# Kernel tuning notes

Measured on AMD Instinct MI355X. Metric: run time of the kernel, lower is better.

The kernel has to match this reference:

```python
import jax, jax.numpy as jnp
import numpy as np

N = 10000
E = 160000
UNITS = 64
NUM_RBF = 32
CUTOFF = 1.0


def _xavier(k, shape):
    fan_out, fan_in = shape
    lim = float(np.sqrt(6.0 / (fan_in + fan_out)))
    return jax.random.uniform(k, shape, minval=-lim, maxval=lim, dtype=jnp.float32)


def setup_inputs() -> dict:
    key = jax.random.key(0)
    ks = jax.random.split(key, 16)
    inp = {
        "edge_index": jax.random.randint(ks[0], (2, E), 0, N),
        "edge_weight": jax.random.uniform(ks[1], (E,), dtype=jnp.float32),
        "edge_attr": jax.random.normal(ks[2], (E, NUM_RBF), dtype=jnp.float32),
        "X": jax.random.normal(ks[3], (N, UNITS, 3, 3), dtype=jnp.float32),
        # scalar MLP: num_rbf -> units -> 2*units -> 3*units
        "Ws0": _xavier(ks[4], (UNITS, NUM_RBF)), "bs0": jnp.zeros((UNITS,), jnp.float32),
        "Ws1": _xavier(ks[5], (2 * UNITS, UNITS)), "bs1": jnp.zeros((2 * UNITS,), jnp.float32),
        "Ws2": _xavier(ks[6], (3 * UNITS, 2 * UNITS)), "bs2": jnp.zeros((3 * UNITS,), jnp.float32),
    }
    for i in range(6):
        inp[f"Wt{i}"] = _xavier(ks[7 + i], (UNITS, UNITS))
    return inp


def cosine_cutoff(r, cutoff):
    return jnp.where(r < cutoff, 0.5 * (jnp.cos(jnp.pi * r / cutoff) + 1.0), 0.0)


def tensor_norm(X):
    # X: [N, units, 3, 3] -> [N, units]
    return jnp.sum(X * X, axis=(-2, -1))


def decompose_tensor(X):
    eye = jnp.eye(3, dtype=X.dtype)
    trace = jnp.trace(X, axis1=-2, axis2=-1)  # [N, units]
    I = (trace / 3.0)[..., None, None] * eye
    A = 0.5 * (X - jnp.swapaxes(X, -2, -1))
    S = 0.5 * (X + jnp.swapaxes(X, -2, -1)) - I
    return I, A, S


def channel_linear(T, W):
    # linear over the channel dim: [N, c, 3, 3] x [d, c] -> [N, d, 3, 3]
    return jnp.einsum('ncij,dc->ndij', T, W)


def reference(edge_index, edge_weight, edge_attr, X,
              Ws0, bs0, Ws1, bs1, Ws2, bs2,
              Wt0, Wt1, Wt2, Wt3, Wt4, Wt5):
    act = jax.nn.silu
    C = cosine_cutoff(edge_weight, CUTOFF)  # [E]
    h = act(edge_attr @ Ws0.T + bs0)
    h = act(h @ Ws1.T + bs1)
    h = act(h @ Ws2.T + bs2)  # [E, 3*units]
    ea = (h * C[:, None]).reshape(h.shape[0], UNITS, 3)  # [E, units, 3]

    X = X / (tensor_norm(X) + 1.0)[..., None, None]
    I, A, S = decompose_tensor(X)
    I = channel_linear(I, Wt0)
    A = channel_linear(A, Wt1)
    S = channel_linear(S, Wt2)
    Y = I + A + S

    src, dst = edge_index[0], edge_index[1]
    n = X.shape[0]
    # message = per-edge radial scaling of gathered node tensors; aggregate at src
    Im = jax.ops.segment_sum(ea[..., 0, None, None] * I[dst], src, num_segments=n)
    Am = jax.ops.segment_sum(ea[..., 1, None, None] * A[dst], src, num_segments=n)
    Sm = jax.ops.segment_sum(ea[..., 2, None, None] * S[dst], src, num_segments=n)
    msg = Im + Am + Sm

    # O(3): symmetrized product of batched 3x3 matmuls
    AB = jnp.matmul(msg, Y) + jnp.matmul(Y, msg)
    I2, A2, S2 = decompose_tensor(AB)
    normp1 = (tensor_norm(I2 + A2 + S2) + 1.0)[..., None, None]
    I2 = channel_linear(I2 / normp1, Wt3)
    A2 = channel_linear(A2 / normp1, Wt4)
    S2 = channel_linear(S2 / normp1, Wt5)
    dX = I2 + A2 + S2
    return X + dX + jnp.matmul(dX, dX)
```

## Files before the change

kernel.cpp:

```cpp
#include <hip/hip_runtime.h>
#include <math.h>

#define NN 10000
#define EE 160000

#define OFF_WTT 0
#define OFF_PK  24576
#define OFF_B2P 41984
#define OFF_IASH 42176
#define OFF_EAH 3242176
#define OFF_INT 18602176

typedef __attribute__((ext_vector_type(8))) _Float16 h16x8;
typedef __attribute__((ext_vector_type(2))) __fp16 fp16x2_raw;
typedef __attribute__((ext_vector_type(4))) float f32x4;

__device__ __forceinline__ float silu_f(float x) {
    return x * __builtin_amdgcn_rcpf(1.0f + __expf(-x));
}
__device__ __forceinline__ unsigned int pkh(float a, float b) {
    union { fp16x2_raw h; unsigned int u; } cv;
    cv.h = __builtin_amdgcn_cvt_pkrtz(a, b);
    return cv.u;
}
__device__ __forceinline__ unsigned short f2h(float f) {
    union { _Float16 h; unsigned short u; } cv; cv.h = (_Float16)f; return cv.u;
}
__device__ __forceinline__ float h2f(unsigned short s) {
    union { unsigned short u; _Float16 h; } cv; cv.u = s; return (float)cv.h;
}
__device__ __forceinline__ float h2f_lo(unsigned int u) { return h2f((unsigned short)(u & 0xffffu)); }
__device__ __forceinline__ float h2f_hi(unsigned int u) { return h2f((unsigned short)(u >> 16)); }

__global__ void k_prep(const float* __restrict__ Wt0, const float* __restrict__ Wt1,
                       const float* __restrict__ Wt2, const float* __restrict__ Wt3,
                       const float* __restrict__ Wt4, const float* __restrict__ Wt5,
                       const float* __restrict__ Ws0, const float* __restrict__ Ws1,
                       const float* __restrict__ Ws2, const float* __restrict__ bs2,
                       const int* __restrict__ ei,
                       float* __restrict__ WtT, unsigned short* __restrict__ PK,
                       float* __restrict__ bs2p, int* __restrict__ counts) {
    int idx = blockIdx.x * 256 + threadIdx.x;
    if (idx < 24576) {
        int k = idx >> 12, r = idx & 4095;
        int c = r >> 6, d = r & 63;
        const float* W = (k == 0) ? Wt0 : (k == 1) ? Wt1 : (k == 2) ? Wt2
                       : (k == 3) ? Wt3 : (k == 4) ? Wt4 : Wt5;
        WtT[idx] = W[d * 64 + c];
    } else if (idx < 26624) {
        int q = idx - 24576;
        int ot = q >> 9, r = q & 511, lane = r >> 3, j = r & 7;
        int k = ((lane >> 4) * 8) + j, o = ot * 16 + (lane & 15);
        PK[q] = f2h(Ws0[o * 32 + k]);
    } else if (idx < 34816) {
        int q = idx - 24576;
        int i = q - 2048, ch = i >> 9, r = i & 511, lane = r >> 3, j = r & 7;
        int ot = ch >> 1, ks = ch & 1;
        int k = ks * 32 + (lane >> 4) * 8 + j, o = ot * 16 + (lane & 15);
        PK[q] = f2h(Ws1[o * 64 + k]);
    } else if (idx < 59392) {
        int q = idx - 24576;
        int i = q - 10240, ch = i >> 9, r = i & 511, lane = r >> 3, j = r & 7;
        int ot = ch >> 2, ks = ch & 3;
        int k = ks * 32 + (lane >> 4) * 8 + j;
        int op = ot * 16 + (lane & 15);
        int o = (op & 63) * 3 + (op >> 6);
        PK[q] = f2h(Ws2[o * 128 + k]);
    } else if (idx < 59584) {
        int op = idx - 59392;
        bs2p[op] = bs2[(op & 63) * 3 + (op >> 6)];
    } else if (idx < 59584 + EE) {
        int e = idx - 59584;
        atomicAdd(&counts[ei[e]], 1);
    }
}

__global__ __launch_bounds__(256) void k_scan(const int* __restrict__ counts,
                                              int* __restrict__ offsets) {
    __shared__ int sums[256];
    int t = threadIdx.x;
    int base = t * 40;
    int s = 0;
    if (base < NN) {
        const int4* p = (const int4*)(counts + base);
#pragma unroll
        for (int q = 0; q < 10; ++q) { int4 a = p[q]; s += a.x + a.y + a.z + a.w; }
    }
    sums[t] = s;
    __syncthreads();
    for (int off = 1; off < 256; off <<= 1) {
        int tmp = (t >= off) ? sums[t - off] : 0;
        __syncthreads();
        sums[t] += tmp;
        __syncthreads();
    }
    int run = sums[t] - s;
    if (base < NN) {
        const int4* p = (const int4*)(counts + base);
#pragma unroll
        for (int q = 0; q < 10; ++q) {
            int4 a = p[q];
            offsets[base + 4 * q + 0] = run; run += a.x;
            offsets[base + 4 * q + 1] = run; run += a.y;
            offsets[base + 4 * q + 2] = run; run += a.z;
            offsets[base + 4 * q + 3] = run; run += a.w;
        }
    }
    if (t == 255) offsets[NN] = run;
}

__global__ void k_fill(const int* __restrict__ ei, const int* __restrict__ offsets,
                       int* __restrict__ cursor, int* __restrict__ bucket,
                       int* __restrict__ dstp) {
    int e = blockIdx.x * 256 + threadIdx.x;
    if (e < EE) {
        int s = ei[e];
        int pos = offsets[s] + atomicAdd(&cursor[s], 1);
        bucket[pos] = e;
        dstp[pos] = ei[EE + e];
    }
}

__global__ __launch_bounds__(256) void k_nodeprep(const float* __restrict__ X,
                                                  const float* __restrict__ WtT,
                                                  unsigned int* __restrict__ IASu) {
    int t = threadIdx.x, w = t >> 6, c = t & 63;
    int n = blockIdx.x * 4 + w;
    __shared__ float XS[4][576];
    __shared__ float L[4][64][12];
    float* xs = XS[w];
#pragma unroll
    for (int i = 0; i < 9; i++) xs[c + 64 * i] = X[(size_t)n * 576 + c + 64 * i];
    __builtin_amdgcn_wave_barrier();
    float x[9];
#pragma unroll
    for (int j = 0; j < 9; j++) x[j] = xs[c * 9 + j];
    float nrm = 0.f;
#pragma unroll
    for (int j = 0; j < 9; j++) nrm += x[j] * x[j];
    float inv = __builtin_amdgcn_rcpf(nrm + 1.0f);
#pragma unroll
    for (int j = 0; j < 9; j++) x[j] *= inv;
    float tr3 = (x[0] + x[4] + x[8]) * (1.0f / 3.0f);
    L[w][c][0] = tr3;
    L[w][c][1] = 0.5f * (x[1] - x[3]);
    L[w][c][2] = 0.5f * (x[2] - x[6]);
    L[w][c][3] = 0.5f * (x[5] - x[7]);
    L[w][c][4] = x[0] - tr3;
    L[w][c][5] = x[4] - tr3;
    L[w][c][6] = 0.5f * (x[1] + x[3]);
    L[w][c][7] = 0.5f * (x[2] + x[6]);
    L[w][c][8] = 0.5f * (x[5] + x[7]);
    __builtin_amdgcn_wave_barrier();
    int d = c;
    const float* W0 = WtT;
    const float* W1 = WtT + 4096;
    const float* W2 = WtT + 8192;
    float aI = 0, aA0 = 0, aA1 = 0, aA2 = 0, aS0 = 0, aS1 = 0, aS2 = 0, aS3 = 0, aS4 = 0;
    for (int cc = 0; cc < 64; ++cc) {
        float w0 = W0[cc * 64 + d], w1 = W1[cc * 64 + d], w2 = W2[cc * 64 + d];
        float4 L0 = *(const float4*)&L[w][cc][0];
        float4 L1 = *(const float4*)&L[w][cc][4];
        float L8 = L[w][cc][8];
        aI  += w0 * L0.x;
        aA0 += w1 * L0.y; aA1 += w1 * L0.z; aA2 += w1 * L0.w;
        aS0 += w2 * L1.x; aS1 += w2 * L1.y; aS2 += w2 * L1.z;
        aS3 += w2 * L1.w; aS4 += w2 * L8;
    }
    unsigned int* op = IASu + (size_t)n * 320 + d;
    op[0]   = pkh(aI, aA0);
    op[64]  = pkh(aA1, aA2);
    op[128] = pkh(aS0, aS1);
    op[192] = pkh(aS2, aS3);
    op[256] = pkh(aS4, 0.0f);
}

__global__ __launch_bounds__(256) void k_mlp(const float* __restrict__ attr,
                                             const float* __restrict__ ew,
                                             const int* __restrict__ bucket,
                                             const unsigned short* __restrict__ PK,
                                             const float* __restrict__ bs0,
                                             const float* __restrict__ bs1,
                                             const float* __restrict__ bs2p,
                                             unsigned short* __restrict__ eah) {
    __shared__ unsigned short H[4][2][16][136];
    int t = threadIdx.x;
    int l = t & 63, w = t >> 6, lr = l & 15, lg = l >> 4;
    int base = blockIdx.x * 128 + w * 32;
    const h16x8* P1 = (const h16x8*)PK;
    const h16x8* P2 = (const h16x8*)(PK + 2048);
    const h16x8* P3 = (const h16x8*)(PK + 10240);

    union { h16x8 h; unsigned int u[4]; } B1[2];
    float C[2];
#pragma unroll
    for (int tt = 0; tt < 2; ++tt) {
        int eid = bucket[base + tt * 16 + lr];
        const float* ap = attr + (size_t)eid * 32 + lg * 8;
        float4 a0 = *(const float4*)ap;
        float4 a1 = *(const float4*)(ap + 4);
        B1[tt].u[0] = pkh(a0.x, a0.y); B1[tt].u[1] = pkh(a0.z, a0.w);
        B1[tt].u[2] = pkh(a1.x, a1.y); B1[tt].u[3] = pkh(a1.z, a1.w);
        float rw = ew[eid];
        C[tt] = (rw < 1.0f) ? 0.5f * (cosf(3.14159265358979f * rw) + 1.0f) : 0.0f;
    }

#pragma unroll
    for (int ot = 0; ot < 4; ++ot) {
        h16x8 wf = P1[ot * 64 + l];
        float4 bb = *(const float4*)&bs0[ot * 16 + lg * 4];
#pragma unroll
        for (int tt = 0; tt < 2; ++tt) {
            f32x4 acc = {bb.x, bb.y, bb.z, bb.w};
            acc = __builtin_amdgcn_mfma_f32_16x16x32_f16(wf, B1[tt].h, acc, 0, 0, 0);
            unsigned int u01 = pkh(silu_f(acc[0]), silu_f(acc[1]));
            unsigned int u23 = pkh(silu_f(acc[2]), silu_f(acc[3]));
            *(uint2*)&H[w][tt][lr][ot * 16 + lg * 4] = make_uint2(u01, u23);
        }
    }
    __builtin_amdgcn_wave_barrier();

    h16x8 B2a[2], B2b[2];
#pragma unroll
    for (int tt = 0; tt < 2; ++tt) {
        B2a[tt] = *(const h16x8*)&H[w][tt][lr][lg * 8];
        B2b[tt] = *(const h16x8*)&H[w][tt][lr][32 + lg * 8];
    }
    __builtin_amdgcn_wave_barrier();
#pragma unroll
    for (int ot = 0; ot < 8; ++ot) {
        h16x8 wf0 = P2[(ot * 2 + 0) * 64 + l];
        h16x8 wf1 = P2[(ot * 2 + 1) * 64 + l];
        float4 bb = *(const float4*)&bs1[ot * 16 + lg * 4];
#pragma unroll
        for (int tt = 0; tt < 2; ++tt) {
            f32x4 acc = {bb.x, bb.y, bb.z, bb.w};
            acc = __builtin_amdgcn_mfma_f32_16x16x32_f16(wf0, B2a[tt], acc, 0, 0, 0);
            acc = __builtin_amdgcn_mfma_f32_16x16x32_f16(wf1, B2b[tt], acc, 0, 0, 0);
            unsigned int u01 = pkh(silu_f(acc[0]), silu_f(acc[1]));
            unsigned int u23 = pkh(silu_f(acc[2]), silu_f(acc[3]));
            *(uint2*)&H[w][tt][lr][ot * 16 + lg * 4] = make_uint2(u01, u23);
        }
    }
    __builtin_amdgcn_wave_barrier();

    h16x8 B3[4][2];
#pragma unroll
    for (int ks = 0; ks < 4; ++ks)
#pragma unroll
        for (int tt = 0; tt < 2; ++tt)
            B3[ks][tt] = *(const h16x8*)&H[w][tt][lr][ks * 32 + lg * 8];
#pragma unroll
    for (int ot = 0; ot < 12; ++ot) {
        h16x8 wf0 = P3[(ot * 4 + 0) * 64 + l];
        h16x8 wf1 = P3[(ot * 4 + 1) * 64 + l];
        h16x8 wf2 = P3[(ot * 4 + 2) * 64 + l];
        h16x8 wf3 = P3[(ot * 4 + 3) * 64 + l];
        float4 bb = *(const float4*)&bs2p[ot * 16 + lg * 4];
#pragma unroll
        for (int tt = 0; tt < 2; ++tt) {
            f32x4 acc = {bb.x, bb.y, bb.z, bb.w};
            acc = __builtin_amdgcn_mfma_f32_16x16x32_f16(wf0, B3[0][tt], acc, 0, 0, 0);
            acc = __builtin_amdgcn_mfma_f32_16x16x32_f16(wf1, B3[1][tt], acc, 0, 0, 0);
            acc = __builtin_amdgcn_mfma_f32_16x16x32_f16(wf2, B3[2][tt], acc, 0, 0, 0);
            acc = __builtin_amdgcn_mfma_f32_16x16x32_f16(wf3, B3[3][tt], acc, 0, 0, 0);
            unsigned int u01 = pkh(silu_f(acc[0]) * C[tt], silu_f(acc[1]) * C[tt]);
            unsigned int u23 = pkh(silu_f(acc[2]) * C[tt], silu_f(acc[3]) * C[tt]);
            *(uint2*)&eah[(size_t)(base + tt * 16 + lr) * 192 + ot * 16 + lg * 4]
                = make_uint2(u01, u23);
        }
    }
}

__global__ __launch_bounds__(256) void k_aggout(const int* __restrict__ offsets,
                                                const int* __restrict__ dstp,
                                                const unsigned short* __restrict__ eah,
                                                const unsigned int* __restrict__ IASu,
                                                const float* __restrict__ X,
                                                const float* __restrict__ WtT,
                                                float* __restrict__ out) {
    int t = threadIdx.x, w = t >> 6, c = t & 63;
    int n = blockIdx.x * 4 + w;
    __shared__ float XS[4][576];
    __shared__ float LO[4][768];
    float* xs = XS[w];
    float* lo = LO[w];
#pragma unroll
    for (int i = 0; i < 9; i++) xs[c + 64 * i] = X[(size_t)n * 576 + c + 64 * i];

    int beg = offsets[n], end = offsets[n + 1];
    float m0 = 0, m1 = 0, m2 = 0, m3 = 0, m4 = 0, m5 = 0, m6 = 0, m7 = 0, m8 = 0;
    int i = beg;
    for (; i + 2 <= end; i += 2) {
        int d0 = dstp[i], d1 = dstp[i + 1];
        const unsigned short* ep0 = eah + (size_t)i * 192;
        const unsigned short* ep1 = ep0 + 192;
        float a00 = h2f(ep0[c]), a01 = h2f(ep0[64 + c]), a02 = h2f(ep0[128 + c]);
        float a10 = h2f(ep1[c]), a11 = h2f(ep1[64 + c]), a12 = h2f(ep1[128 + c]);
        const unsigned int* p0 = IASu + (size_t)d0 * 320 + c;
        const unsigned int* p1 = IASu + (size_t)d1 * 320 + c;
        unsigned int u00 = p0[0], u01 = p0[64], u02 = p0[128], u03 = p0[192], u04 = p0[256];
        unsigned int u10 = p1[0], u11 = p1[64], u12 = p1[128], u13 = p1[192], u14 = p1[256];
        m0 += a00 * h2f_lo(u00) + a10 * h2f_lo(u10);
        m1 += a01 * h2f_hi(u00) + a11 * h2f_hi(u10);
        m2 += a01 * h2f_lo(u01) + a11 * h2f_lo(u11);
        m3 += a01 * h2f_hi(u01) + a11 * h2f_hi(u11);
        m4 += a02 * h2f_lo(u02) + a12 * h2f_lo(u12);
        m5 += a02 * h2f_hi(u02) + a12 * h2f_hi(u12);
        m6 += a02 * h2f_lo(u03) + a12 * h2f_lo(u13);
        m7 += a02 * h2f_hi(u03) + a12 * h2f_hi(u13);
        m8 += a02 * h2f_lo(u04) + a12 * h2f_lo(u14);
    }
    if (i < end) {
        int d0 = dstp[i];
        const unsigned short* ep0 = eah + (size_t)i * 192;
        float a00 = h2f(ep0[c]), a01 = h2f(ep0[64 + c]), a02 = h2f(ep0[128 + c]);
        const unsigned int* p0 = IASu + (size_t)d0 * 320 + c;
        unsigned int u00 = p0[0], u01 = p0[64], u02 = p0[128], u03 = p0[192], u04 = p0[256];
        m0 += a00 * h2f_lo(u00); m1 += a01 * h2f_hi(u00);
        m2 += a01 * h2f_lo(u01); m3 += a01 * h2f_hi(u01);
        m4 += a02 * h2f_lo(u02); m5 += a02 * h2f_hi(u02);
        m6 += a02 * h2f_lo(u03); m7 += a02 * h2f_hi(u03);
        m8 += a02 * h2f_lo(u04);
    }
    const unsigned int* yp = IASu + (size_t)n * 320 + c;
    unsigned int y0 = yp[0], y1 = yp[64], y2 = yp[128], y3 = yp[192], y4 = yp[256];
    float yI = h2f_lo(y0), yA0 = h2f_hi(y0), yA1 = h2f_lo(y1), yA2 = h2f_hi(y1);
    float yS0 = h2f_lo(y2), yS1 = h2f_hi(y2), yS2 = h2f_lo(y3), yS3 = h2f_hi(y3);
    float yS4 = h2f_lo(y4);

    float M[3][3] = {
        { m0 + m4,   m1 + m6,  m2 + m7 },
        { -m1 + m6,  m0 + m5,  m3 + m8 },
        { -m2 + m7, -m3 + m8,  m0 - m4 - m5 } };
    float Y[3][3] = {
        { yI + yS0,   yA0 + yS2,  yA1 + yS3 },
        { -yA0 + yS2, yI + yS1,   yA2 + yS4 },
        { -yA1 + yS3, -yA2 + yS4, yI - yS0 - yS1 } };
    float AB[3][3];
#pragma unroll
    for (int ii = 0; ii < 3; ii++)
#pragma unroll
        for (int j = 0; j < 3; j++) {
            float s = 0.f;
#pragma unroll
            for (int k = 0; k < 3; k++) s += M[ii][k] * Y[k][j] + Y[ii][k] * M[k][j];
            AB[ii][j] = s;
        }
    float tr3 = (AB[0][0] + AB[1][1] + AB[2][2]) * (1.0f / 3.0f);
    float fro = 0.f;
#pragma unroll
    for (int ii = 0; ii < 3; ii++)
#pragma unroll
        for (int j = 0; j < 3; j++) fro += AB[ii][j] * AB[ii][j];
    float inv = __builtin_amdgcn_rcpf(fro + 1.0f);
    float (*L12)[12] = (float (*)[12])lo;
    L12[c][0] = tr3 * inv;
    L12[c][1] = 0.5f * (AB[0][1] - AB[1][0]) * inv;
    L12[c][2] = 0.5f * (AB[0][2] - AB[2][0]) * inv;
    L12[c][3] = 0.5f * (AB[1][2] - AB[2][1]) * inv;
    L12[c][4] = (AB[0][0] - tr3) * inv;
    L12[c][5] = (AB[1][1] - tr3) * inv;
    L12[c][6] = 0.5f * (AB[0][1] + AB[1][0]) * inv;
    L12[c][7] = 0.5f * (AB[0][2] + AB[2][0]) * inv;
    L12[c][8] = 0.5f * (AB[1][2] + AB[2][1]) * inv;
    __builtin_amdgcn_wave_barrier();
    int d = c;
    const float* W3 = WtT + 3 * 4096;
    const float* W4 = WtT + 4 * 4096;
    const float* W5 = WtT + 5 * 4096;
    float aI = 0, aA0 = 0, aA1 = 0, aA2 = 0, aS0 = 0, aS1 = 0, aS2 = 0, aS3 = 0, aS4 = 0;
    for (int cc = 0; cc < 64; ++cc) {
        float w3 = W3[cc * 64 + d], w4 = W4[cc * 64 + d], w5 = W5[cc * 64 + d];
        float4 L0 = *(const float4*)&L12[cc][0];
        float4 L1 = *(const float4*)&L12[cc][4];
        float L8 = L12[cc][8];
        aI  += w3 * L0.x;
        aA0 += w4 * L0.y; aA1 += w4 * L0.z; aA2 += w4 * L0.w;
        aS0 += w5 * L1.x; aS1 += w5 * L1.y; aS2 += w5 * L1.z;
        aS3 += w5 * L1.w; aS4 += w5 * L8;
    }
    float dX[3][3] = {
        { aI + aS0,   aA0 + aS2,  aA1 + aS3 },
        { -aA0 + aS2, aI + aS1,   aA2 + aS4 },
        { -aA1 + aS3, -aA2 + aS4, aI - aS0 - aS1 } };
    float D2[3][3];
#pragma unroll
    for (int ii = 0; ii < 3; ii++)
#pragma unroll
        for (int j = 0; j < 3; j++) {
            float s = 0.f;
#pragma unroll
            for (int k = 0; k < 3; k++) s += dX[ii][k] * dX[k][j];
            D2[ii][j] = s;
        }
    float x[9];
    __builtin_amdgcn_wave_barrier();
#pragma unroll
    for (int j = 0; j < 9; j++) x[j] = xs[d * 9 + j];
    float nrm = 0.f;
#pragma unroll
    for (int j = 0; j < 9; j++) nrm += x[j] * x[j];
    float xinv = __builtin_amdgcn_rcpf(nrm + 1.0f);
    __builtin_amdgcn_wave_barrier();
#pragma unroll
    for (int ii = 0; ii < 3; ii++)
#pragma unroll
        for (int j = 0; j < 3; j++)
            lo[d * 9 + ii * 3 + j] = x[ii * 3 + j] * xinv + dX[ii][j] + D2[ii][j];
    __builtin_amdgcn_wave_barrier();
#pragma unroll
    for (int ii = 0; ii < 9; ii++) out[(size_t)n * 576 + c + 64 * ii] = lo[c + 64 * ii];
}

extern "C" void kernel_launch(void* const* d_in, const int* in_sizes, int n_in,
                              void* d_out, int out_size, void* d_ws, size_t ws_size,
                              hipStream_t stream) {
    (void)in_sizes; (void)n_in; (void)out_size; (void)ws_size;
    const int* ei = (const int*)d_in[0];
    const float* ew = (const float*)d_in[1];
    const float* attr = (const float*)d_in[2];
    const float* X = (const float*)d_in[3];
    const float* Ws0 = (const float*)d_in[4];
    const float* bs0 = (const float*)d_in[5];
    const float* Ws1 = (const float*)d_in[6];
    const float* bs1 = (const float*)d_in[7];
    const float* Ws2 = (const float*)d_in[8];
    const float* bs2 = (const float*)d_in[9];
    const float* Wt0 = (const float*)d_in[10];
    const float* Wt1 = (const float*)d_in[11];
    const float* Wt2 = (const float*)d_in[12];
    const float* Wt3 = (const float*)d_in[13];
    const float* Wt4 = (const float*)d_in[14];
    const float* Wt5 = (const float*)d_in[15];
    float* ws = (float*)d_ws;
    int* ibase = (int*)(ws + OFF_INT);
    int* counts = ibase;
    int* cursor = ibase + NN;
    int* offsets = ibase + 2 * NN;
    int* bucket = ibase + 3 * NN + 1;
    int* dstp = bucket + EE;
    unsigned short* PK = (unsigned short*)(ws + OFF_PK);
    unsigned int* IASu = (unsigned int*)(ws + OFF_IASH);
    unsigned short* eah = (unsigned short*)(ws + OFF_EAH);

    (void)hipMemsetAsync(counts, 0, 2 * NN * sizeof(int), stream);
    k_prep<<<(59584 + EE + 255) / 256, 256, 0, stream>>>(
        Wt0, Wt1, Wt2, Wt3, Wt4, Wt5, Ws0, Ws1, Ws2, bs2, ei,
        ws, PK, ws + OFF_B2P, counts);
    k_scan<<<1, 256, 0, stream>>>(counts, offsets);
    k_fill<<<(EE + 255) / 256, 256, 0, stream>>>(ei, offsets, cursor, bucket, dstp);
    k_nodeprep<<<NN / 4, 256, 0, stream>>>(X, ws, IASu);
    k_mlp<<<EE / 128, 256, 0, stream>>>(attr, ew, bucket, PK, bs0, bs1, ws + OFF_B2P, eah);
    k_aggout<<<NN / 4, 256, 0, stream>>>(offsets, dstp, eah, IASu, X, ws, (float*)d_out);
}
```

Baseline: 151.5 us.

## Permute edge attrs in fill, merge nodeprep into MLP kernel, unroll aggregation by 4

The fill kernel now writes fp16-packed edge attributes and the cosine cutoff directly in bucket-sorted order, so the MLP reads contiguous rows instead of gathering through a bucket index. The node-prep work becomes extra blocks of the MLP launch, which saves one kernel launch and lets the two independent stages share the GPU. The aggregation loop is unrolled by four so more gathers are in flight at once. In exchange, fill does more scattered writes and the workspace holds an extra permuted attribute buffer.

```diff
diff --git a/kernel.cpp b/kernel.cpp
--- a/kernel.cpp
+++ b/kernel.cpp
@@ -9,7 +9,9 @@
 #define OFF_B2P 41984
 #define OFF_IASH 42176
 #define OFF_EAH 3242176
-#define OFF_INT 18602176
+#define OFF_ATTRP 18602176
+#define OFF_CP  21162176
+#define OFF_INT 21322176
 
 typedef __attribute__((ext_vector_type(8))) _Float16 h16x8;
 typedef __attribute__((ext_vector_type(2))) __fp16 fp16x2_raw;
@@ -110,165 +112,170 @@
 }
 
 __global__ void k_fill(const int* __restrict__ ei, const int* __restrict__ offsets,
-                       int* __restrict__ cursor, int* __restrict__ bucket,
-                       int* __restrict__ dstp) {
+                       const float* __restrict__ attr, const float* __restrict__ ew,
+                       int* __restrict__ cursor, int* __restrict__ dstp,
+                       unsigned short* __restrict__ attrP, float* __restrict__ Cp) {
     int e = blockIdx.x * 256 + threadIdx.x;
     if (e < EE) {
         int s = ei[e];
         int pos = offsets[s] + atomicAdd(&cursor[s], 1);
-        bucket[pos] = e;
         dstp[pos] = ei[EE + e];
-    }
-}
-
-__global__ __launch_bounds__(256) void k_nodeprep(const float* __restrict__ X,
-                                                  const float* __restrict__ WtT,
-                                                  unsigned int* __restrict__ IASu) {
-    int t = threadIdx.x, w = t >> 6, c = t & 63;
-    int n = blockIdx.x * 4 + w;
-    __shared__ float XS[4][576];
-    __shared__ float L[4][64][12];
-    float* xs = XS[w];
-#pragma unroll
-    for (int i = 0; i < 9; i++) xs[c + 64 * i] = X[(size_t)n * 576 + c + 64 * i];
-    __builtin_amdgcn_wave_barrier();
-    float x[9];
-#pragma unroll
-    for (int j = 0; j < 9; j++) x[j] = xs[c * 9 + j];
-    float nrm = 0.f;
-#pragma unroll
-    for (int j = 0; j < 9; j++) nrm += x[j] * x[j];
-    float inv = __builtin_amdgcn_rcpf(nrm + 1.0f);
-#pragma unroll
-    for (int j = 0; j < 9; j++) x[j] *= inv;
-    float tr3 = (x[0] + x[4] + x[8]) * (1.0f / 3.0f);
-    L[w][c][0] = tr3;
-    L[w][c][1] = 0.5f * (x[1] - x[3]);
-    L[w][c][2] = 0.5f * (x[2] - x[6]);
-    L[w][c][3] = 0.5f * (x[5] - x[7]);
-    L[w][c][4] = x[0] - tr3;
-    L[w][c][5] = x[4] - tr3;
-    L[w][c][6] = 0.5f * (x[1] + x[3]);
-    L[w][c][7] = 0.5f * (x[2] + x[6]);
-    L[w][c][8] = 0.5f * (x[5] + x[7]);
-    __builtin_amdgcn_wave_barrier();
-    int d = c;
-    const float* W0 = WtT;
-    const float* W1 = WtT + 4096;
-    const float* W2 = WtT + 8192;
-    float aI = 0, aA0 = 0, aA1 = 0, aA2 = 0, aS0 = 0, aS1 = 0, aS2 = 0, aS3 = 0, aS4 = 0;
-    for (int cc = 0; cc < 64; ++cc) {
-        float w0 = W0[cc * 64 + d], w1 = W1[cc * 64 + d], w2 = W2[cc * 64 + d];
-        float4 L0 = *(const float4*)&L[w][cc][0];
-        float4 L1 = *(const float4*)&L[w][cc][4];
-        float L8 = L[w][cc][8];
-        aI  += w0 * L0.x;
-        aA0 += w1 * L0.y; aA1 += w1 * L0.z; aA2 += w1 * L0.w;
-        aS0 += w2 * L1.x; aS1 += w2 * L1.y; aS2 += w2 * L1.z;
-        aS3 += w2 * L1.w; aS4 += w2 * L8;
-    }
-    unsigned int* op = IASu + (size_t)n * 320 + d;
-    op[0]   = pkh(aI, aA0);
-    op[64]  = pkh(aA1, aA2);
-    op[128] = pkh(aS0, aS1);
-    op[192] = pkh(aS2, aS3);
-    op[256] = pkh(aS4, 0.0f);
-}
-
-__global__ __launch_bounds__(256) void k_mlp(const float* __restrict__ attr,
-                                             const float* __restrict__ ew,
-                                             const int* __restrict__ bucket,
-                                             const unsigned short* __restrict__ PK,
-                                             const float* __restrict__ bs0,
-                                             const float* __restrict__ bs1,
-                                             const float* __restrict__ bs2p,
-                                             unsigned short* __restrict__ eah) {
-    __shared__ unsigned short H[4][2][16][136];
-    int t = threadIdx.x;
-    int l = t & 63, w = t >> 6, lr = l & 15, lg = l >> 4;
-    int base = blockIdx.x * 128 + w * 32;
-    const h16x8* P1 = (const h16x8*)PK;
-    const h16x8* P2 = (const h16x8*)(PK + 2048);
-    const h16x8* P3 = (const h16x8*)(PK + 10240);
-
-    union { h16x8 h; unsigned int u[4]; } B1[2];
-    float C[2];
-#pragma unroll
-    for (int tt = 0; tt < 2; ++tt) {
-        int eid = bucket[base + tt * 16 + lr];
-        const float* ap = attr + (size_t)eid * 32 + lg * 8;
-        float4 a0 = *(const float4*)ap;
-        float4 a1 = *(const float4*)(ap + 4);
-        B1[tt].u[0] = pkh(a0.x, a0.y); B1[tt].u[1] = pkh(a0.z, a0.w);
-        B1[tt].u[2] = pkh(a1.x, a1.y); B1[tt].u[3] = pkh(a1.z, a1.w);
-        float rw = ew[eid];
-        C[tt] = (rw < 1.0f) ? 0.5f * (cosf(3.14159265358979f * rw) + 1.0f) : 0.0f;
-    }
-
-#pragma unroll
-    for (int ot = 0; ot < 4; ++ot) {
-        h16x8 wf = P1[ot * 64 + l];
-        float4 bb = *(const float4*)&bs0[ot * 16 + lg * 4];
+        const float4* ap = (const float4*)(attr + (size_t)e * 32);
+        unsigned int pk[16];
+#pragma unroll
+        for (int q = 0; q < 8; ++q) {
+            float4 v = ap[q];
+            pk[2 * q]     = pkh(v.x, v.y);
+            pk[2 * q + 1] = pkh(v.z, v.w);
+        }
+        uint4* dst = (uint4*)(attrP + (size_t)pos * 32);
+#pragma unroll
+        for (int q = 0; q < 4; ++q)
+            dst[q] = make_uint4(pk[4 * q], pk[4 * q + 1], pk[4 * q + 2], pk[4 * q + 3]);
+        float rw = ew[e];
+        Cp[pos] = (rw < 1.0f) ? 0.5f * (cosf(3.14159265358979f * rw) + 1.0f) : 0.0f;
+    }
+}
+
+__global__ __launch_bounds__(256) void k_mlpnp(const unsigned short* __restrict__ attrP,
+                                               const float* __restrict__ Cp,
+                                               const unsigned short* __restrict__ PK,
+                                               const float* __restrict__ bs0,
+                                               const float* __restrict__ bs1,
+                                               const float* __restrict__ bs2p,
+                                               const float* __restrict__ X,
+                                               const float* __restrict__ WtT,
+                                               unsigned short* __restrict__ eah,
+                                               unsigned int* __restrict__ IASu) {
+    __shared__ unsigned short SH[4][4352];
+    int t = threadIdx.x, w = t >> 6, l = t & 63;
+    if (blockIdx.x < EE / 128) {
+        int lr = l & 15, lg = l >> 4;
+        int base = blockIdx.x * 128 + w * 32;
+        unsigned short* Hh = SH[w];
+        const h16x8* P1 = (const h16x8*)PK;
+        const h16x8* P2 = (const h16x8*)(PK + 2048);
+        const h16x8* P3 = (const h16x8*)(PK + 10240);
+        union { h16x8 h; uint4 v; } B1[2];
+        float C[2];
 #pragma unroll
         for (int tt = 0; tt < 2; ++tt) {
-            f32x4 acc = {bb.x, bb.y, bb.z, bb.w};
-            acc = __builtin_amdgcn_mfma_f32_16x16x32_f16(wf, B1[tt].h, acc, 0, 0, 0);
-            unsigned int u01 = pkh(silu_f(acc[0]), silu_f(acc[1]));
-            unsigned int u23 = pkh(silu_f(acc[2]), silu_f(acc[3]));
-            *(uint2*)&H[w][tt][lr][ot * 16 + lg * 4] = make_uint2(u01, u23);
-        }
-    }
-    __builtin_amdgcn_wave_barrier();
-
-    h16x8 B2a[2], B2b[2];
-#pragma unroll
-    for (int tt = 0; tt < 2; ++tt) {
-        B2a[tt] = *(const h16x8*)&H[w][tt][lr][lg * 8];
-        B2b[tt] = *(const h16x8*)&H[w][tt][lr][32 + lg * 8];
-    }
-    __builtin_amdgcn_wave_barrier();
-#pragma unroll
-    for (int ot = 0; ot < 8; ++ot) {
-        h16x8 wf0 = P2[(ot * 2 + 0) * 64 + l];
-        h16x8 wf1 = P2[(ot * 2 + 1) * 64 + l];
-        float4 bb = *(const float4*)&bs1[ot * 16 + lg * 4];
+            int p = base + tt * 16 + lr;
+            B1[tt].v = *((const uint4*)(attrP + (size_t)p * 32) + lg);
+            C[tt] = Cp[p];
+        }
+#pragma unroll
+        for (int ot = 0; ot < 4; ++ot) {
+            h16x8 wf = P1[ot * 64 + l];
+            float4 bb = *(const float4*)&bs0[ot * 16 + lg * 4];
+#pragma unroll
+            for (int tt = 0; tt < 2; ++tt) {
+                f32x4 acc = {bb.x, bb.y, bb.z, bb.w};
+                acc = __builtin_amdgcn_mfma_f32_16x16x32_f16(wf, B1[tt].h, acc, 0, 0, 0);
+                unsigned int u01 = pkh(silu_f(acc[0]), silu_f(acc[1]));
+                unsigned int u23 = pkh(silu_f(acc[2]), silu_f(acc[3]));
+                *(uint2*)&Hh[tt * 2176 + lr * 136 + ot * 16 + lg * 4] = make_uint2(u01, u23);
+            }
+        }
+        __builtin_amdgcn_wave_barrier();
+        h16x8 B2a[2], B2b[2];
 #pragma unroll
         for (int tt = 0; tt < 2; ++tt) {
-            f32x4 acc = {bb.x, bb.y, bb.z, bb.w};
-            acc = __builtin_amdgcn_mfma_f32_16x16x32_f16(wf0, B2a[tt], acc, 0, 0, 0);
-            acc = __builtin_amdgcn_mfma_f32_16x16x32_f16(wf1, B2b[tt], acc, 0, 0, 0);
-            unsigned int u01 = pkh(silu_f(acc[0]), silu_f(acc[1]));
-            unsigned int u23 = pkh(silu_f(acc[2]), silu_f(acc[3]));
-            *(uint2*)&H[w][tt][lr][ot * 16 + lg * 4] = make_uint2(u01, u23);
-        }
-    }
-    __builtin_amdgcn_wave_barrier();
-
-    h16x8 B3[4][2];
-#pragma unroll
-    for (int ks = 0; ks < 4; ++ks)
-#pragma unroll
-        for (int tt = 0; tt < 2; ++tt)
-            B3[ks][tt] = *(const h16x8*)&H[w][tt][lr][ks * 32 + lg * 8];
-#pragma unroll
-    for (int ot = 0; ot < 12; ++ot) {
-        h16x8 wf0 = P3[(ot * 4 + 0) * 64 + l];
-        h16x8 wf1 = P3[(ot * 4 + 1) * 64 + l];
-        h16x8 wf2 = P3[(ot * 4 + 2) * 64 + l];
-        h16x8 wf3 = P3[(ot * 4 + 3) * 64 + l];
-        float4 bb = *(const float4*)&bs2p[ot * 16 + lg * 4];
-#pragma unroll
-        for (int tt = 0; tt < 2; ++tt) {
-            f32x4 acc = {bb.x, bb.y, bb.z, bb.w};
-            acc = __builtin_amdgcn_mfma_f32_16x16x32_f16(wf0, B3[0][tt], acc, 0, 0, 0);
-            acc = __builtin_amdgcn_mfma_f32_16x16x32_f16(wf1, B3[1][tt], acc, 0, 0, 0);
-            acc = __builtin_amdgcn_mfma_f32_16x16x32_f16(wf2, B3[2][tt], acc, 0, 0, 0);
-            acc = __builtin_amdgcn_mfma_f32_16x16x32_f16(wf3, B3[3][tt], acc, 0, 0, 0);
-            unsigned int u01 = pkh(silu_f(acc[0]) * C[tt], silu_f(acc[1]) * C[tt]);
-            unsigned int u23 = pkh(silu_f(acc[2]) * C[tt], silu_f(acc[3]) * C[tt]);
-            *(uint2*)&eah[(size_t)(base + tt * 16 + lr) * 192 + ot * 16 + lg * 4]
-                = make_uint2(u01, u23);
-        }
+            B2a[tt] = *(const h16x8*)&Hh[tt * 2176 + lr * 136 + lg * 8];
+            B2b[tt] = *(const h16x8*)&Hh[tt * 2176 + lr * 136 + 32 + lg * 8];
+        }
+        __builtin_amdgcn_wave_barrier();
+#pragma unroll
+        for (int ot = 0; ot < 8; ++ot) {
+            h16x8 wf0 = P2[(ot * 2 + 0) * 64 + l];
+            h16x8 wf1 = P2[(ot * 2 + 1) * 64 + l];
+            float4 bb = *(const float4*)&bs1[ot * 16 + lg * 4];
+#pragma unroll
+            for (int tt = 0; tt < 2; ++tt) {
+                f32x4 acc = {bb.x, bb.y, bb.z, bb.w};
+                acc = __builtin_amdgcn_mfma_f32_16x16x32_f16(wf0, B2a[tt], acc, 0, 0, 0);
+                acc = __builtin_amdgcn_mfma_f32_16x16x32_f16(wf1, B2b[tt], acc, 0, 0, 0);
+                unsigned int u01 = pkh(silu_f(acc[0]), silu_f(acc[1]));
+                unsigned int u23 = pkh(silu_f(acc[2]), silu_f(acc[3]));
+                *(uint2*)&Hh[tt * 2176 + lr * 136 + ot * 16 + lg * 4] = make_uint2(u01, u23);
+            }
+        }
+        __builtin_amdgcn_wave_barrier();
+        h16x8 B3[4][2];
+#pragma unroll
+        for (int ks = 0; ks < 4; ++ks)
+#pragma unroll
+            for (int tt = 0; tt < 2; ++tt)
+                B3[ks][tt] = *(const h16x8*)&Hh[tt * 2176 + lr * 136 + ks * 32 + lg * 8];
+#pragma unroll
+        for (int ot = 0; ot < 12; ++ot) {
+            h16x8 wf0 = P3[(ot * 4 + 0) * 64 + l];
+            h16x8 wf1 = P3[(ot * 4 + 1) * 64 + l];
+            h16x8 wf2 = P3[(ot * 4 + 2) * 64 + l];
+            h16x8 wf3 = P3[(ot * 4 + 3) * 64 + l];
+            float4 bb = *(const float4*)&bs2p[ot * 16 + lg * 4];
+#pragma unroll
+            for (int tt = 0; tt < 2; ++tt) {
+                f32x4 acc = {bb.x, bb.y, bb.z, bb.w};
+                acc = __builtin_amdgcn_mfma_f32_16x16x32_f16(wf0, B3[0][tt], acc, 0, 0, 0);
+                acc = __builtin_amdgcn_mfma_f32_16x16x32_f16(wf1, B3[1][tt], acc, 0, 0, 0);
+                acc = __builtin_amdgcn_mfma_f32_16x16x32_f16(wf2, B3[2][tt], acc, 0, 0, 0);
+                acc = __builtin_amdgcn_mfma_f32_16x16x32_f16(wf3, B3[3][tt], acc, 0, 0, 0);
+                unsigned int u01 = pkh(silu_f(acc[0]) * C[tt], silu_f(acc[1]) * C[tt]);
+                unsigned int u23 = pkh(silu_f(acc[2]) * C[tt], silu_f(acc[3]) * C[tt]);
+                *(uint2*)&eah[(size_t)(base + tt * 16 + lr) * 192 + ot * 16 + lg * 4]
+                    = make_uint2(u01, u23);
+            }
+        }
+    } else {
+        int c = l;
+        int n = (blockIdx.x - EE / 128) * 4 + w;
+        float* xs = (float*)SH[w];
+        float (*L12)[12] = (float (*)[12])(xs + 576);
+#pragma unroll
+        for (int i = 0; i < 9; i++) xs[c + 64 * i] = X[(size_t)n * 576 + c + 64 * i];
+        __builtin_amdgcn_wave_barrier();
+        float x[9];
+#pragma unroll
+        for (int j = 0; j < 9; j++) x[j] = xs[c * 9 + j];
+        float nrm = 0.f;
+#pragma unroll
+        for (int j = 0; j < 9; j++) nrm += x[j] * x[j];
+        float inv = __builtin_amdgcn_rcpf(nrm + 1.0f);
+#pragma unroll
+        for (int j = 0; j < 9; j++) x[j] *= inv;
+        float tr3 = (x[0] + x[4] + x[8]) * (1.0f / 3.0f);
+        L12[c][0] = tr3;
+        L12[c][1] = 0.5f * (x[1] - x[3]);
+        L12[c][2] = 0.5f * (x[2] - x[6]);
+        L12[c][3] = 0.5f * (x[5] - x[7]);
+        L12[c][4] = x[0] - tr3;
+        L12[c][5] = x[4] - tr3;
+        L12[c][6] = 0.5f * (x[1] + x[3]);
+        L12[c][7] = 0.5f * (x[2] + x[6]);
+        L12[c][8] = 0.5f * (x[5] + x[7]);
+        __builtin_amdgcn_wave_barrier();
+        int d = c;
+        const float* W0 = WtT;
+        const float* W1 = WtT + 4096;
+        const float* W2 = WtT + 8192;
+        float aI = 0, aA0 = 0, aA1 = 0, aA2 = 0, aS0 = 0, aS1 = 0, aS2 = 0, aS3 = 0, aS4 = 0;
+        for (int cc = 0; cc < 64; ++cc) {
+            float w0 = W0[cc * 64 + d], w1 = W1[cc * 64 + d], w2 = W2[cc * 64 + d];
+            float4 L0 = *(const float4*)&L12[cc][0];
+            float4 L1 = *(const float4*)&L12[cc][4];
+            float L8 = L12[cc][8];
+            aI  += w0 * L0.x;
+            aA0 += w1 * L0.y; aA1 += w1 * L0.z; aA2 += w1 * L0.w;
+            aS0 += w2 * L1.x; aS1 += w2 * L1.y; aS2 += w2 * L1.z;
+            aS3 += w2 * L1.w; aS4 += w2 * L8;
+        }
+        unsigned int* op = IASu + (size_t)n * 320 + d;
+        op[0]   = pkh(aI, aA0);
+        op[64]  = pkh(aA1, aA2);
+        op[128] = pkh(aS0, aS1);
+        op[192] = pkh(aS2, aS3);
+        op[256] = pkh(aS4, 0.0f);
     }
 }
 
@@ -291,37 +298,35 @@
     int beg = offsets[n], end = offsets[n + 1];
     float m0 = 0, m1 = 0, m2 = 0, m3 = 0, m4 = 0, m5 = 0, m6 = 0, m7 = 0, m8 = 0;
     int i = beg;
-    for (; i + 2 <= end; i += 2) {
-        int d0 = dstp[i], d1 = dstp[i + 1];
-        const unsigned short* ep0 = eah + (size_t)i * 192;
-        const unsigned short* ep1 = ep0 + 192;
-        float a00 = h2f(ep0[c]), a01 = h2f(ep0[64 + c]), a02 = h2f(ep0[128 + c]);
-        float a10 = h2f(ep1[c]), a11 = h2f(ep1[64 + c]), a12 = h2f(ep1[128 + c]);
-        const unsigned int* p0 = IASu + (size_t)d0 * 320 + c;
-        const unsigned int* p1 = IASu + (size_t)d1 * 320 + c;
-        unsigned int u00 = p0[0], u01 = p0[64], u02 = p0[128], u03 = p0[192], u04 = p0[256];
-        unsigned int u10 = p1[0], u11 = p1[64], u12 = p1[128], u13 = p1[192], u14 = p1[256];
-        m0 += a00 * h2f_lo(u00) + a10 * h2f_lo(u10);
-        m1 += a01 * h2f_hi(u00) + a11 * h2f_hi(u10);
-        m2 += a01 * h2f_lo(u01) + a11 * h2f_lo(u11);
-        m3 += a01 * h2f_hi(u01) + a11 * h2f_hi(u11);
-        m4 += a02 * h2f_lo(u02) + a12 * h2f_lo(u12);
-        m5 += a02 * h2f_hi(u02) + a12 * h2f_hi(u12);
-        m6 += a02 * h2f_lo(u03) + a12 * h2f_lo(u13);
-        m7 += a02 * h2f_hi(u03) + a12 * h2f_hi(u13);
-        m8 += a02 * h2f_lo(u04) + a12 * h2f_lo(u14);
-    }
-    if (i < end) {
-        int d0 = dstp[i];
-        const unsigned short* ep0 = eah + (size_t)i * 192;
-        float a00 = h2f(ep0[c]), a01 = h2f(ep0[64 + c]), a02 = h2f(ep0[128 + c]);
-        const unsigned int* p0 = IASu + (size_t)d0 * 320 + c;
-        unsigned int u00 = p0[0], u01 = p0[64], u02 = p0[128], u03 = p0[192], u04 = p0[256];
-        m0 += a00 * h2f_lo(u00); m1 += a01 * h2f_hi(u00);
-        m2 += a01 * h2f_lo(u01); m3 += a01 * h2f_hi(u01);
-        m4 += a02 * h2f_lo(u02); m5 += a02 * h2f_hi(u02);
-        m6 += a02 * h2f_lo(u03); m7 += a02 * h2f_hi(u03);
-        m8 += a02 * h2f_lo(u04);
+    for (; i + 4 <= end; i += 4) {
+        float a[4][3];
+        unsigned int u[4][5];
+#pragma unroll
+        for (int q = 0; q < 4; ++q) {
+            const unsigned short* ep = eah + (size_t)(i + q) * 192;
+            a[q][0] = h2f(ep[c]); a[q][1] = h2f(ep[64 + c]); a[q][2] = h2f(ep[128 + c]);
+            const unsigned int* p = IASu + (size_t)dstp[i + q] * 320 + c;
+            u[q][0] = p[0]; u[q][1] = p[64]; u[q][2] = p[128]; u[q][3] = p[192]; u[q][4] = p[256];
+        }
+#pragma unroll
+        for (int q = 0; q < 4; ++q) {
+            m0 += a[q][0] * h2f_lo(u[q][0]); m1 += a[q][1] * h2f_hi(u[q][0]);
+            m2 += a[q][1] * h2f_lo(u[q][1]); m3 += a[q][1] * h2f_hi(u[q][1]);
+            m4 += a[q][2] * h2f_lo(u[q][2]); m5 += a[q][2] * h2f_hi(u[q][2]);
+            m6 += a[q][2] * h2f_lo(u[q][3]); m7 += a[q][2] * h2f_hi(u[q][3]);
+            m8 += a[q][2] * h2f_lo(u[q][4]);
+        }
+    }
+    for (; i < end; ++i) {
+        const unsigned short* ep = eah + (size_t)i * 192;
+        float a0 = h2f(ep[c]), a1 = h2f(ep[64 + c]), a2 = h2f(ep[128 + c]);
+        const unsigned int* p = IASu + (size_t)dstp[i] * 320 + c;
+        unsigned int u0 = p[0], u1 = p[64], u2 = p[128], u3 = p[192], u4 = p[256];
+        m0 += a0 * h2f_lo(u0); m1 += a1 * h2f_hi(u0);
+        m2 += a1 * h2f_lo(u1); m3 += a1 * h2f_hi(u1);
+        m4 += a2 * h2f_lo(u2); m5 += a2 * h2f_hi(u2);
+        m6 += a2 * h2f_lo(u3); m7 += a2 * h2f_hi(u3);
+        m8 += a2 * h2f_lo(u4);
     }
     const unsigned int* yp = IASu + (size_t)n * 320 + c;
     unsigned int y0 = yp[0], y1 = yp[64], y2 = yp[128], y3 = yp[192], y4 = yp[256];
@@ -438,19 +443,20 @@
     int* counts = ibase;
     int* cursor = ibase + NN;
     int* offsets = ibase + 2 * NN;
-    int* bucket = ibase + 3 * NN + 1;
-    int* dstp = bucket + EE;
+    int* dstp = ibase + 3 * NN + 1;
     unsigned short* PK = (unsigned short*)(ws + OFF_PK);
     unsigned int* IASu = (unsigned int*)(ws + OFF_IASH);
     unsigned short* eah = (unsigned short*)(ws + OFF_EAH);
+    unsigned short* attrP = (unsigned short*)(ws + OFF_ATTRP);
+    float* Cp = ws + OFF_CP;
 
     (void)hipMemsetAsync(counts, 0, 2 * NN * sizeof(int), stream);
     k_prep<<<(59584 + EE + 255) / 256, 256, 0, stream>>>(
         Wt0, Wt1, Wt2, Wt3, Wt4, Wt5, Ws0, Ws1, Ws2, bs2, ei,
         ws, PK, ws + OFF_B2P, counts);
     k_scan<<<1, 256, 0, stream>>>(counts, offsets);
-    k_fill<<<(EE + 255) / 256, 256, 0, stream>>>(ei, offsets, cursor, bucket, dstp);
-    k_nodeprep<<<NN / 4, 256, 0, stream>>>(X, ws, IASu);
-    k_mlp<<<EE / 128, 256, 0, stream>>>(attr, ew, bucket, PK, bs0, bs1, ws + OFF_B2P, eah);
+    k_fill<<<(EE + 255) / 256, 256, 0, stream>>>(ei, offsets, attr, ew, cursor, dstp, attrP, Cp);
+    k_mlpnp<<<EE / 128 + NN / 4, 256, 0, stream>>>(attrP, Cp, PK, bs0, bs1, ws + OFF_B2P,
+                                                   X, ws, eah, IASu);
     k_aggout<<<NN / 4, 256, 0, stream>>>(offsets, dstp, eah, IASu, X, ws, (float*)d_out);
 }
```

After: 150.3 us. No clear change (-0.8%).
